# Kernel optimization log

Hardware: AMD Instinct MI355X
Metric: run time of the kernel (lower is better)

The kernel has to match this reference:

```python
import jax, jax.numpy as jnp
import numpy as np
from jax import lax

NX = 4096
NY = 4096
NLEVEL = 13  # int(log2(min(nx, ny))) + 1
OMEGA = 1.0
DN = ('NCHW', 'OIHW', 'NCHW')


def _bc(u):
    # torch boundary_condition: replicate edges into a zero-padded frame; corners stay 0
    up = jnp.pad(u, ((0, 0), (0, 0), (1, 1), (1, 1)), mode='edge')
    up = up.at[0, 0, 0, 0].set(0.0)
    up = up.at[0, 0, 0, -1].set(0.0)
    up = up.at[0, 0, -1, 0].set(0.0)
    up = up.at[0, 0, -1, -1].set(0.0)
    return up


def _prol(x):
    return jnp.repeat(jnp.repeat(x, 2, axis=2), 2, axis=3)


def setup_inputs() -> dict:
    key = jax.random.key(0)
    k1, k2 = jax.random.split(key)
    # realistic 5-point-like stencil with strong diagonal + randn perturbation
    base = jnp.array([[0.0, 1.0, 0.0], [1.0, 4.0, 1.0], [0.0, 1.0, 0.0]], dtype=jnp.float32)
    A = base + 0.01 * jax.random.normal(k1, (3, 3), dtype=jnp.float32)
    u0 = jax.random.normal(k2, (1, 1, NY, NX), dtype=jnp.float32)
    return {"A": A, "u0": u0, "t": 4}


def reference(A, u0, t):
    diag = A[1, 1]                      # center extracted before zeroing, as in __init__
    K = (A.at[1, 1].set(0.0))[None, None]  # (1,1,3,3) smoothing kernel, zero center
    KR = jnp.full((1, 1, 2, 2), 0.25, dtype=A.dtype)  # restriction kernel

    def smooth(x):
        return lax.conv_general_dilated(x, K, (1, 1), 'VALID', dimension_numbers=DN)

    def restrict(x):
        return lax.conv_general_dilated(x, KR, (2, 2), 'VALID', dimension_numbers=DN)

    b = 0.0
    u = u0
    for _ in range(t):
        r = smooth(_bc(u)) - b  # (1,1,NY,NX)
        r_s = [r]
        for _i in range(1, NLEVEL - 5):
            r = restrict(r)
            r_s.append(r)
        e = jnp.zeros((1, 1, 1, 1), dtype=A.dtype)
        for j in reversed(range(1, NLEVEL - 5)):
            e_pad = jnp.pad(e, ((0, 0), (0, 0), (1, 1), (1, 1)))
            e = e - smooth(e_pad) / diag + r_s[j] / diag  # broadcasts to r_s[j] shape
            e = _prol(e)
        u_update = u - e - smooth(_bc(u)) / diag + b / diag
        u = (1.0 - OMEGA) * u + OMEGA * u_update
    return (u - u.min()) / (u.max() - u.min())
```

## Files before the change

kernel.cpp:

```cpp
#include <hip/hip_runtime.h>

#define N 4096

__device__ __forceinline__ float bf2f(unsigned short h)
{
    unsigned int u = ((unsigned int)h) << 16;
    return __uint_as_float(u);
}
__device__ __forceinline__ unsigned short f2bf(float f)
{
    unsigned int x = __float_as_uint(f);
    unsigned int r = (x + 0x7FFFu + ((x >> 16) & 1u)) >> 16;
    return (unsigned short)r;
}

__device__ __forceinline__ int cr(int i) { return ((i + 1024) >> 1) - 512; }

__device__ __forceinline__ void load_A(const float* __restrict__ Ag,
                                       float Ac[3][3], float& inv)
{
#pragma unroll
    for (int i = 0; i < 9; ++i) Ac[i / 3][i % 3] = Ag[i];
    inv = 1.0f / Ac[1][1];
    Ac[1][1] = 0.f;
}

__device__ __forceinline__ void make_w44(const float Ac[3][3], float wt[4][4])
{
#pragma unroll
    for (int a = 0; a < 4; ++a)
#pragma unroll
        for (int b = 0; b < 4; ++b) wt[a][b] = 0.f;
#pragma unroll
    for (int r = 0; r < 2; ++r)
#pragma unroll
        for (int c = 0; c < 2; ++c)
#pragma unroll
            for (int i = 0; i < 3; ++i)
#pragma unroll
                for (int j = 0; j < 3; ++j) wt[r + i][c + j] += Ac[i][j];
}

template <typename TI>
__device__ __forceinline__ void load_row6T(const TI* __restrict__ u,
                                           int gy, int xm, int colL, int colR,
                                           bool cornL, bool cornR, bool yedge,
                                           float v[6])
{
    int cy = min(max(gy, 0), N - 1);
    const TI* rowp = &u[(size_t)cy * N];
    float L, R;
    if constexpr (sizeof(TI) == 4) {
        float4 m = *(const float4*)&rowp[xm];
        v[1] = m.x; v[2] = m.y; v[3] = m.z; v[4] = m.w;
        L = rowp[colL];
        R = rowp[colR];
    } else {
        ushort4 m = *(const ushort4*)&rowp[xm];
        v[1] = bf2f(m.x); v[2] = bf2f(m.y); v[3] = bf2f(m.z); v[4] = bf2f(m.w);
        L = bf2f(rowp[colL]);
        R = bf2f(rowp[colR]);
    }
    if (yedge) {
        bool oob = (gy < 0) | (gy >= N);
        if (oob & cornL) L = 0.f;
        if (oob & cornR) R = 0.f;
    }
    v[0] = L; v[5] = R;
}

__device__ __forceinline__ void swz2048(int bid, int& bx, int& by)
{
    int reg = (bid & 7) * 256 + (bid >> 3);
    bx = reg & 15;
    by = reg >> 4;
}

template <typename TI>
__global__ __launch_bounds__(256) void smooth_restrict2_kernel(
    const TI* __restrict__ u, const float* __restrict__ Ag,
    unsigned short* __restrict__ r2, float* __restrict__ r3)
{
    int t = threadIdx.x, lane = t & 63, w = t >> 6;
    int bx, by;
    swz2048(blockIdx.x, bx, by);
    int x0 = 256 * bx;
    int Y0 = 16 * by + 4 * w;
    int gy0 = 2 * Y0 - 1;
    bool yedge = (gy0 < 0) | (gy0 + 9 >= N);
    float Ac[3][3], inv;
    load_A(Ag, Ac, inv);
    float wt[4][4];
    make_w44(Ac, wt);

    int xm = x0 + 4 * lane;
    int colL = max(xm - 1, 0), colR = min(xm + 4, N - 1);
    bool cornL = (xm - 1 < 0), cornR = (xm + 4 >= N);
    float v[10][6];
#pragma unroll
    for (int rr = 0; rr < 10; ++rr)
        load_row6T<TI>(u, gy0 + rr, xm, colL, colR, cornL, cornR, yedge, v[rr]);

    float o0[4], o1[4];
#pragma unroll
    for (int q = 0; q < 4; ++q) {
        float a0 = 0.f, a1 = 0.f;
#pragma unroll
        for (int a = 0; a < 4; ++a) {
            const float* vv = v[2 * q + a];
#pragma unroll
            for (int b = 0; b < 4; ++b) {
                a0 += wt[a][b] * vv[b];
                a1 += wt[a][b] * vv[b + 2];
            }
        }
        o0[q] = 0.25f * a0;
        o1[q] = 0.25f * a1;
    }
    int Y2 = Y0 >> 1, X2 = 64 * bx + lane;
    float val0 = 0.25f * (o0[0] + o1[0] + o0[1] + o1[1]);
    float val1 = 0.25f * (o0[2] + o1[2] + o0[3] + o1[3]);
    r2[(size_t)Y2 * 1024 + X2] = f2bf(val0);
    r2[(size_t)(Y2 + 1) * 1024 + X2] = f2bf(val1);
    float s0 = val0 + val1;
    float s1 = __shfl_xor(s0, 1);
    if (!(lane & 1))
        r3[(size_t)(Y2 >> 1) * 512 + (X2 >> 1)] = 0.25f * (s0 + s1);
}

__global__ __launch_bounds__(256) void multirestrict_kernel(
    const float* __restrict__ r3, float* __restrict__ r4, float* __restrict__ r5,
    float* __restrict__ r6, float* __restrict__ r7)
{
    int BX = blockIdx.x, BY = blockIdx.y;
    __shared__ float s4[16][17];
    __shared__ float s5[8][9];
    __shared__ float s6[4][5];
    int t = threadIdx.x;
    {
        int y = t >> 4, x = t & 15;
        const float* b0 = &r3[(size_t)(32 * BY + 2 * y) * 512 + 32 * BX + 2 * x];
        float2 a = *(const float2*)b0;
        float2 b = *(const float2*)(b0 + 512);
        float vv = 0.25f * (a.x + a.y + b.x + b.y);
        r4[(size_t)(16 * BY + y) * 256 + 16 * BX + x] = vv;
        s4[y][x] = vv;
    }
    __syncthreads();
    if (t < 64) {
        int y = t >> 3, x = t & 7;
        float vv = 0.25f * (s4[2 * y][2 * x] + s4[2 * y][2 * x + 1] +
                            s4[2 * y + 1][2 * x] + s4[2 * y + 1][2 * x + 1]);
        r5[(size_t)(8 * BY + y) * 128 + 8 * BX + x] = vv;
        s5[y][x] = vv;
    }
    __syncthreads();
    if (t < 16) {
        int y = t >> 2, x = t & 3;
        float vv = 0.25f * (s5[2 * y][2 * x] + s5[2 * y][2 * x + 1] +
                            s5[2 * y + 1][2 * x] + s5[2 * y + 1][2 * x + 1]);
        r6[(size_t)(4 * BY + y) * 64 + 4 * BX + x] = vv;
        s6[y][x] = vv;
    }
    __syncthreads();
    if (t < 4) {
        int y = t >> 1, x = t & 1;
        float vv = 0.25f * (s6[2 * y][2 * x] + s6[2 * y][2 * x + 1] +
                            s6[2 * y + 1][2 * x] + s6[2 * y + 1][2 * x + 1]);
        r7[(size_t)(2 * BY + y) * 32 + 2 * BX + x] = vv;
    }
}

template <typename TI, typename TO, bool WANTMM>
__global__ __launch_bounds__(256) void final_fused_kernel(
    const TI* __restrict__ u,
    const float* __restrict__ r7, const float* __restrict__ r6,
    const float* __restrict__ r5, const float* __restrict__ r4,
    const float* __restrict__ r3, const unsigned short* __restrict__ r2,
    const float* __restrict__ Ag, TO* __restrict__ uo,
    float* __restrict__ partials)
{
    const int n = N;
    int t = threadIdx.x, lane = t & 63, w = t >> 6;
    int bx, by;
    swz2048(blockIdx.x, bx, by);
    int x0 = 256 * bx, y0 = 32 * by;
    __shared__ float s32p[3][4];
    __shared__ float s64p[3][6];
    __shared__ float s128p[3][10];
    __shared__ float s256p[4][18];
    __shared__ float s512v[6][36];
    __shared__ float s1024[10][68];
    float Ac[3][3], inv;
    load_A(Ag, Ac, inv);
    float wt[4][4];
    make_w44(Ac, wt);

    int yb = y0 + 8 * w;
    int gyu = yb - 1;
    bool yedge = (gyu < 0) | (gyu + 9 >= n);
    int xm = x0 + 4 * lane;
    int colL = max(xm - 1, 0), colR = min(xm + 4, n - 1);
    bool cornL = (xm - 1 < 0), cornR = (xm + 4 >= n);
    float v[10][6];
#pragma unroll
    for (int rr = 0; rr < 10; ++rr)
        load_row6T<TI>(u, gyu + rr, xm, colL, colR, cornL, cornR, yedge, v[rr]);

    int R32 = (by >> 2) - 1, C32 = 2 * bx - 1;
    if (t < 12) {
        int pr = t >> 2, pc = t & 3;
        int gy = R32 + pr, gx = C32 + pc;
        s32p[pr][pc] = (gy >= 0 && gy < 32 && gx >= 0 && gx < 32)
                           ? r7[(size_t)gy * 32 + gx] * inv : 0.f;
    }
    __syncthreads();
    int R64 = (by >> 1) - 1, C64 = 4 * bx - 1;
    if (t < 18) {
        int pr = t / 6, pc = t - (t / 6) * 6;
        int gy = R64 + pr, gx = C64 + pc;
        float val = 0.f;
        if (gy >= 0 && gy < 64 && gx >= 0 && gx < 64) {
            float ctr = s32p[cr(gy) - R32][cr(gx) - C32];
            float sm = 0.f;
#pragma unroll
            for (int dy = -1; dy <= 1; ++dy)
#pragma unroll
                for (int dx = -1; dx <= 1; ++dx) {
                    if (dy == 0 && dx == 0) continue;
                    sm += Ac[dy + 1][dx + 1] * s32p[cr(gy + dy) - R32][cr(gx + dx) - C32];
                }
            val = ctr - sm * inv + r6[(size_t)gy * 64 + gx] * inv;
        }
        s64p[pr][pc] = val;
    }
    __syncthreads();
    int R128 = by - 1, C128 = 8 * bx - 1;
    if (t < 30) {
        int pr = t / 10, pc = t - (t / 10) * 10;
        int gy = R128 + pr, gx = C128 + pc;
        float val = 0.f;
        if (gy >= 0 && gy < 128 && gx >= 0 && gx < 128) {
            float ctr = s64p[cr(gy) - R64][cr(gx) - C64];
            float sm = 0.f;
#pragma unroll
            for (int dy = -1; dy <= 1; ++dy)
#pragma unroll
                for (int dx = -1; dx <= 1; ++dx) {
                    if (dy == 0 && dx == 0) continue;
                    sm += Ac[dy + 1][dx + 1] * s64p[cr(gy + dy) - R64][cr(gx + dx) - C64];
                }
            val = ctr - sm * inv + r5[(size_t)gy * 128 + gx] * inv;
        }
        s128p[pr][pc] = val;
    }
    __syncthreads();
    int R256 = 2 * by - 1, C256 = 16 * bx - 1;
    if (t < 72) {
        int pr = t / 18, pc = t - (t / 18) * 18;
        int gy = R256 + pr, gx = C256 + pc;
        float val = 0.f;
        if (gy >= 0 && gy < 256 && gx >= 0 && gx < 256) {
            float ctr = s128p[cr(gy) - R128][cr(gx) - C128];
            float sm = 0.f;
#pragma unroll
            for (int dy = -1; dy <= 1; ++dy)
#pragma unroll
                for (int dx = -1; dx <= 1; ++dx) {
                    if (dy == 0 && dx == 0) continue;
                    sm += Ac[dy + 1][dx + 1] * s128p[cr(gy + dy) - R128][cr(gx + dx) - C128];
                }
            val = ctr - sm * inv + r4[(size_t)gy * 256 + gx] * inv;
        }
        s256p[pr][pc] = val;
    }
    __syncthreads();
    int S5r = 4 * by - 1, S5c = 32 * bx - 1;
    if (t < 216) {
        int pr = t / 36, pc = t - (t / 36) * 36;
        int gy = S5r + pr, gx = S5c + pc;
        float val = 0.f;
        if (pc < 34 && gy >= 0 && gy < 512 && gx >= 0 && gx < 512) {
            float ctr = s256p[cr(gy) - R256][cr(gx) - C256];
            float sm = 0.f;
#pragma unroll
            for (int dy = -1; dy <= 1; ++dy)
#pragma unroll
                for (int dx = -1; dx <= 1; ++dx) {
                    if (dy == 0 && dx == 0) continue;
                    sm += Ac[dy + 1][dx + 1] * s256p[cr(gy + dy) - R256][cr(gx + dx) - C256];
                }
            val = ctr - sm * inv + r3[(size_t)gy * 512 + gx] * inv;
        }
        s512v[pr][pc] = val;
    }
    __syncthreads();
    int R10 = 8 * by - 1, C10 = 64 * bx - 1;
    for (int i = t; i < 680; i += 256) {
        int pr = i / 68, pc = i - (i / 68) * 68;
        if (pc < 66) {
            int gy = R10 + pr, gx = C10 + pc;
            float val = 0.f;
            if (gy >= 0 && gy < 1024 && gx >= 0 && gx < 1024) {
                float ctr = s512v[cr(gy) - S5r][cr(gx) - S5c];
                float sm = 0.f;
#pragma unroll
                for (int dy = -1; dy <= 1; ++dy)
#pragma unroll
                    for (int dx = -1; dx <= 1; ++dx) {
                        if (dy == 0 && dx == 0) continue;
                        sm += Ac[dy + 1][dx + 1] *
                              s512v[cr(gy + dy) - S5r][cr(gx + dx) - S5c];
                    }
                val = ctr - sm * inv + bf2f(r2[(size_t)gy * 1024 + gx]) * inv;
            }
            s1024[pr][pc] = val;
        }
    }
    __syncthreads();
    float e2[4][2];
    int EY0 = 16 * by + 4 * w, EX0 = 128 * bx + 2 * lane;
#pragma unroll
    for (int a = 0; a < 4; ++a) {
        int gy = EY0 + a;
        float a0 = 0.f, a1 = 0.f;
#pragma unroll
        for (int i = 0; i < 4; ++i) {
            const float* vv = v[2 * a + i];
#pragma unroll
            for (int j = 0; j < 4; ++j) {
                a0 += wt[i][j] * vv[j];
                a1 += wt[i][j] * vv[j + 2];
            }
        }
        float r1v[2] = {0.25f * a0, 0.25f * a1};
#pragma unroll
        for (int b = 0; b < 2; ++b) {
            int gx = EX0 + b;
            float ctr = s1024[(gy >> 1) - R10][(gx >> 1) - C10];
            float sm = 0.f;
#pragma unroll
            for (int dy = -1; dy <= 1; ++dy)
#pragma unroll
                for (int dx = -1; dx <= 1; ++dx) {
                    if (dy == 0 && dx == 0) continue;
                    sm += Ac[dy + 1][dx + 1] *
                          s1024[((gy + dy) >> 1) - R10][((gx + dx) >> 1) - C10];
                }
            e2[a][b] = ctr - sm * inv + r1v[b] * inv;
        }
    }
    float mn = 3.402823466e+38f, mx = -3.402823466e+38f;
#pragma unroll
    for (int r = 0; r < 8; ++r) {
        int y = yb + r;
        const float* va = v[r];
        const float* vb = v[r + 1];
        const float* vc = v[r + 2];
        float out[4];
#pragma unroll
        for (int c = 0; c < 4; ++c) {
            float sm = Ac[0][0] * va[c] + Ac[0][1] * va[c + 1] + Ac[0][2] * va[c + 2]
                     + Ac[1][0] * vb[c]                        + Ac[1][2] * vb[c + 2]
                     + Ac[2][0] * vc[c] + Ac[2][1] * vc[c + 1] + Ac[2][2] * vc[c + 2];
            out[c] = vb[c + 1] - e2[r >> 1][c >> 1] - sm * inv;
        }
        if constexpr (sizeof(TO) == 4) {
            *(float4*)&uo[(size_t)y * n + xm] =
                make_float4(out[0], out[1], out[2], out[3]);
        } else {
            ushort4 o;
            o.x = f2bf(out[0]); o.y = f2bf(out[1]);
            o.z = f2bf(out[2]); o.w = f2bf(out[3]);
            *(ushort4*)&uo[(size_t)y * n + xm] = o;
        }
        if (WANTMM) {
            mn = fminf(mn, fminf(fminf(out[0], out[1]), fminf(out[2], out[3])));
            mx = fmaxf(mx, fmaxf(fmaxf(out[0], out[1]), fmaxf(out[2], out[3])));
        }
    }
    if (WANTMM) {
#pragma unroll
        for (int off = 32; off > 0; off >>= 1) {
            mn = fminf(mn, __shfl_down(mn, off));
            mx = fmaxf(mx, __shfl_down(mx, off));
        }
        __shared__ float smn[4], smx[4];
        if (lane == 0) { smn[w] = mn; smx[w] = mx; }
        __syncthreads();
        if (t == 0) {
            mn = smn[0]; mx = smx[0];
            for (int wq = 1; wq < 4; ++wq) { mn = fminf(mn, smn[wq]); mx = fmaxf(mx, smx[wq]); }
            int bid = by * 16 + bx;
            partials[2 * bid] = mn;
            partials[2 * bid + 1] = mx;
        }
    }
}

__global__ __launch_bounds__(1024) void minmax_final_kernel(
    const float* __restrict__ partials, float* __restrict__ mm)
{
    float mn = 3.402823466e+38f, mx = -3.402823466e+38f;
    for (int i = threadIdx.x; i < 2048; i += 1024) {
        mn = fminf(mn, partials[2 * i]);
        mx = fmaxf(mx, partials[2 * i + 1]);
    }
#pragma unroll
    for (int off = 32; off > 0; off >>= 1) {
        mn = fminf(mn, __shfl_down(mn, off));
        mx = fmaxf(mx, __shfl_down(mx, off));
    }
    __shared__ float smn[16], smx[16];
    int lane = threadIdx.x & 63, wv = threadIdx.x >> 6;
    if (lane == 0) { smn[wv] = mn; smx[wv] = mx; }
    __syncthreads();
    if (threadIdx.x == 0) {
        mn = smn[0]; mx = smx[0];
        for (int w = 1; w < 16; ++w) { mn = fminf(mn, smn[w]); mx = fmaxf(mx, smx[w]); }
        mm[0] = mn;
        mm[1] = mx;
    }
}

__global__ __launch_bounds__(256) void normalize_kernel(
    const unsigned short* __restrict__ uin, float* __restrict__ uout,
    const float* __restrict__ mm)
{
    size_t i = ((size_t)blockIdx.x * 256 + threadIdx.x) * 4;
    float mn = mm[0];
    float sc = 1.0f / (mm[1] - mm[0]);
    ushort4 h = *(const ushort4*)&uin[i];
    float4 v;
    v.x = (bf2f(h.x) - mn) * sc;
    v.y = (bf2f(h.y) - mn) * sc;
    v.z = (bf2f(h.z) - mn) * sc;
    v.w = (bf2f(h.w) - mn) * sc;
    *(float4*)&uout[i] = v;
}

extern "C" void kernel_launch(void* const* d_in, const int* in_sizes, int n_in,
                              void* d_out, int out_size, void* d_ws, size_t ws_size,
                              hipStream_t stream)
{
    const float* A  = (const float*)d_in[0];
    const float* u0 = (const float*)d_in[1];
    float* uout = (float*)d_out;
    char* ws = (char*)d_ws;

    size_t off = 0;
    auto alloc_f = [&](size_t nelem) { float* p = (float*)(ws + off); off += nelem * 4; return p; };
    float* r3 = alloc_f(512ull * 512);
    float* r4 = alloc_f(256ull * 256);
    float* r5 = alloc_f(128ull * 128);
    float* r6 = alloc_f(64ull * 64);
    float* r7 = alloc_f(32ull * 32);
    float* partials = alloc_f(4096);
    float* mm = alloc_f(2);
    off = (off + 15) & ~15ull;
    unsigned short* r2 = (unsigned short*)(ws + off); off += 1024ull * 1024 * 2;
    off = (off + 15) & ~15ull;
    unsigned short* ubA = (unsigned short*)(ws + off); off += 4096ull * 4096 * 2;
    unsigned short* ubB = (unsigned short*)(ws + off); off += 4096ull * 4096 * 2;

    for (int it = 0; it < 4; ++it) {
        if (it == 0) {
            smooth_restrict2_kernel<float><<<2048, 256, 0, stream>>>(u0, A, r2, r3);
        } else {
            const unsigned short* us = (it == 2) ? ubB : ubA;
            smooth_restrict2_kernel<unsigned short><<<2048, 256, 0, stream>>>(us, A, r2, r3);
        }
        multirestrict_kernel<<<dim3(16, 16), 256, 0, stream>>>(r3, r4, r5, r6, r7);
        if (it == 0) {
            final_fused_kernel<float, unsigned short, false><<<2048, 256, 0, stream>>>(
                u0, r7, r6, r5, r4, r3, r2, A, ubA, partials);
        } else if (it == 1) {
            final_fused_kernel<unsigned short, unsigned short, false><<<2048, 256, 0, stream>>>(
                ubA, r7, r6, r5, r4, r3, r2, A, ubB, partials);
        } else if (it == 2) {
            final_fused_kernel<unsigned short, unsigned short, false><<<2048, 256, 0, stream>>>(
                ubB, r7, r6, r5, r4, r3, r2, A, ubA, partials);
        } else {
            final_fused_kernel<unsigned short, unsigned short, true><<<2048, 256, 0, stream>>>(
                ubA, r7, r6, r5, r4, r3, r2, A, ubB, partials);
        }
    }
    minmax_final_kernel<<<1, 1024, 0, stream>>>(partials, mm);
    normalize_kernel<<<16384, 256, 0, stream>>>(ubB, uout, mm);
}
```

Baseline: 175.4 us.

## Fuse multi-level restriction into final kernel and merge minmax into normalize

Removes the separate multirestrict kernel: each final_fused block now loads a 48x64 halo tile of r3 into shared memory and recomputes r4..r7 locally, reading coarse residuals from LDS instead of global buffers. Also folds the single-block minmax reduction into the normalize kernel, where each block reduces the 2048 partials itself and then processes 8192 elements. The goal is to cut two kernel launches and their serialization per run. In exchange, every block does redundant restriction work, adds several more barriers, and uses more shared memory, which may lower occupancy.

New measurement: 182.5 us. 4.0% more time.

```diff
diff --git a/kernel.cpp b/kernel.cpp
--- a/kernel.cpp
+++ b/kernel.cpp
@@ -128,63 +128,21 @@
         r3[(size_t)(Y2 >> 1) * 512 + (X2 >> 1)] = 0.25f * (s0 + s1);
 }
 
-__global__ __launch_bounds__(256) void multirestrict_kernel(
-    const float* __restrict__ r3, float* __restrict__ r4, float* __restrict__ r5,
-    float* __restrict__ r6, float* __restrict__ r7)
-{
-    int BX = blockIdx.x, BY = blockIdx.y;
-    __shared__ float s4[16][17];
-    __shared__ float s5[8][9];
-    __shared__ float s6[4][5];
-    int t = threadIdx.x;
-    {
-        int y = t >> 4, x = t & 15;
-        const float* b0 = &r3[(size_t)(32 * BY + 2 * y) * 512 + 32 * BX + 2 * x];
-        float2 a = *(const float2*)b0;
-        float2 b = *(const float2*)(b0 + 512);
-        float vv = 0.25f * (a.x + a.y + b.x + b.y);
-        r4[(size_t)(16 * BY + y) * 256 + 16 * BX + x] = vv;
-        s4[y][x] = vv;
-    }
-    __syncthreads();
-    if (t < 64) {
-        int y = t >> 3, x = t & 7;
-        float vv = 0.25f * (s4[2 * y][2 * x] + s4[2 * y][2 * x + 1] +
-                            s4[2 * y + 1][2 * x] + s4[2 * y + 1][2 * x + 1]);
-        r5[(size_t)(8 * BY + y) * 128 + 8 * BX + x] = vv;
-        s5[y][x] = vv;
-    }
-    __syncthreads();
-    if (t < 16) {
-        int y = t >> 2, x = t & 3;
-        float vv = 0.25f * (s5[2 * y][2 * x] + s5[2 * y][2 * x + 1] +
-                            s5[2 * y + 1][2 * x] + s5[2 * y + 1][2 * x + 1]);
-        r6[(size_t)(4 * BY + y) * 64 + 4 * BX + x] = vv;
-        s6[y][x] = vv;
-    }
-    __syncthreads();
-    if (t < 4) {
-        int y = t >> 1, x = t & 1;
-        float vv = 0.25f * (s6[2 * y][2 * x] + s6[2 * y][2 * x + 1] +
-                            s6[2 * y + 1][2 * x] + s6[2 * y + 1][2 * x + 1]);
-        r7[(size_t)(2 * BY + y) * 32 + 2 * BX + x] = vv;
-    }
-}
-
 template <typename TI, typename TO, bool WANTMM>
 __global__ __launch_bounds__(256) void final_fused_kernel(
-    const TI* __restrict__ u,
-    const float* __restrict__ r7, const float* __restrict__ r6,
-    const float* __restrict__ r5, const float* __restrict__ r4,
-    const float* __restrict__ r3, const unsigned short* __restrict__ r2,
-    const float* __restrict__ Ag, TO* __restrict__ uo,
-    float* __restrict__ partials)
+    const TI* __restrict__ u, const float* __restrict__ r3,
+    const unsigned short* __restrict__ r2, const float* __restrict__ Ag,
+    TO* __restrict__ uo, float* __restrict__ partials)
 {
     const int n = N;
     int t = threadIdx.x, lane = t & 63, w = t >> 6;
     int bx, by;
     swz2048(blockIdx.x, bx, by);
     int x0 = 256 * bx, y0 = 32 * by;
+    __shared__ float sr3[48][66];
+    __shared__ float sr4[24][33];
+    __shared__ float sr5[12][17];
+    __shared__ float sr6[6][9];
     __shared__ float s32p[3][4];
     __shared__ float s64p[3][6];
     __shared__ float s128p[3][10];
@@ -207,12 +165,51 @@
     for (int rr = 0; rr < 10; ++rr)
         load_row6T<TI>(u, gyu + rr, xm, colL, colR, cornL, cornR, yedge, v[rr]);
 
+    int R3r = 16 * (by >> 2) - 16, R3c = 32 * bx - 16;
+    {
+        bool interior = (R3r >= 0) & (R3r + 48 <= 512) & (R3c >= 0) & (R3c + 64 <= 512);
+        if (interior) {
+            for (int i = t; i < 1536; i += 256) {
+                int rr = i >> 5, cc = (i & 31) * 2;
+                *(float2*)&sr3[rr][cc] =
+                    *(const float2*)&r3[(size_t)(R3r + rr) * 512 + R3c + cc];
+            }
+        } else {
+            for (int i = t; i < 3072; i += 256) {
+                int rr = i >> 6, cc = i & 63;
+                int gy = R3r + rr, gx = R3c + cc;
+                sr3[rr][cc] = (gy >= 0 && gy < 512 && gx >= 0 && gx < 512)
+                                  ? r3[(size_t)gy * 512 + gx] : 0.f;
+            }
+        }
+    }
+    __syncthreads();
+    int R4r = 8 * (by >> 2) - 8, R4c = 16 * bx - 8;
+    for (int i = t; i < 768; i += 256) {
+        int y = i >> 5, x = i & 31;
+        sr4[y][x] = 0.25f * (sr3[2 * y][2 * x] + sr3[2 * y][2 * x + 1] +
+                             sr3[2 * y + 1][2 * x] + sr3[2 * y + 1][2 * x + 1]);
+    }
+    __syncthreads();
+    int R5r = 4 * (by >> 2) - 4, R5c = 8 * bx - 4;
+    if (t < 192) {
+        int y = t >> 4, x = t & 15;
+        sr5[y][x] = 0.25f * (sr4[2 * y][2 * x] + sr4[2 * y][2 * x + 1] +
+                             sr4[2 * y + 1][2 * x] + sr4[2 * y + 1][2 * x + 1]);
+    }
+    __syncthreads();
+    int R6r = 2 * (by >> 2) - 2, R6c = 4 * bx - 2;
+    if (t < 48) {
+        int y = t >> 3, x = t & 7;
+        sr6[y][x] = 0.25f * (sr5[2 * y][2 * x] + sr5[2 * y][2 * x + 1] +
+                             sr5[2 * y + 1][2 * x] + sr5[2 * y + 1][2 * x + 1]);
+    }
+    __syncthreads();
     int R32 = (by >> 2) - 1, C32 = 2 * bx - 1;
     if (t < 12) {
-        int pr = t >> 2, pc = t & 3;
-        int gy = R32 + pr, gx = C32 + pc;
-        s32p[pr][pc] = (gy >= 0 && gy < 32 && gx >= 0 && gx < 32)
-                           ? r7[(size_t)gy * 32 + gx] * inv : 0.f;
+        int y = t >> 2, x = t & 3;
+        s32p[y][x] = 0.25f * (sr6[2 * y][2 * x] + sr6[2 * y][2 * x + 1] +
+                              sr6[2 * y + 1][2 * x] + sr6[2 * y + 1][2 * x + 1]) * inv;
     }
     __syncthreads();
     int R64 = (by >> 1) - 1, C64 = 4 * bx - 1;
@@ -230,7 +227,7 @@
                     if (dy == 0 && dx == 0) continue;
                     sm += Ac[dy + 1][dx + 1] * s32p[cr(gy + dy) - R32][cr(gx + dx) - C32];
                 }
-            val = ctr - sm * inv + r6[(size_t)gy * 64 + gx] * inv;
+            val = ctr - sm * inv + sr6[gy - R6r][gx - R6c] * inv;
         }
         s64p[pr][pc] = val;
     }
@@ -250,7 +247,7 @@
                     if (dy == 0 && dx == 0) continue;
                     sm += Ac[dy + 1][dx + 1] * s64p[cr(gy + dy) - R64][cr(gx + dx) - C64];
                 }
-            val = ctr - sm * inv + r5[(size_t)gy * 128 + gx] * inv;
+            val = ctr - sm * inv + sr5[gy - R5r][gx - R5c] * inv;
         }
         s128p[pr][pc] = val;
     }
@@ -270,7 +267,7 @@
                     if (dy == 0 && dx == 0) continue;
                     sm += Ac[dy + 1][dx + 1] * s128p[cr(gy + dy) - R128][cr(gx + dx) - C128];
                 }
-            val = ctr - sm * inv + r4[(size_t)gy * 256 + gx] * inv;
+            val = ctr - sm * inv + sr4[gy - R4r][gx - R4c] * inv;
         }
         s256p[pr][pc] = val;
     }
@@ -290,7 +287,7 @@
                     if (dy == 0 && dx == 0) continue;
                     sm += Ac[dy + 1][dx + 1] * s256p[cr(gy + dy) - R256][cr(gx + dx) - C256];
                 }
-            val = ctr - sm * inv + r3[(size_t)gy * 512 + gx] * inv;
+            val = ctr - sm * inv + sr3[gy - R3r][gx - R3c] * inv;
         }
         s512v[pr][pc] = val;
     }
@@ -398,11 +395,13 @@
     }
 }
 
-__global__ __launch_bounds__(1024) void minmax_final_kernel(
-    const float* __restrict__ partials, float* __restrict__ mm)
-{
+__global__ __launch_bounds__(256) void normalize_kernel(
+    const unsigned short* __restrict__ uin, float* __restrict__ uout,
+    const float* __restrict__ partials)
+{
+    int t = threadIdx.x, lane = t & 63, w = t >> 6;
     float mn = 3.402823466e+38f, mx = -3.402823466e+38f;
-    for (int i = threadIdx.x; i < 2048; i += 1024) {
+    for (int i = t; i < 2048; i += 256) {
         mn = fminf(mn, partials[2 * i]);
         mx = fmaxf(mx, partials[2 * i + 1]);
     }
@@ -411,32 +410,30 @@
         mn = fminf(mn, __shfl_down(mn, off));
         mx = fmaxf(mx, __shfl_down(mx, off));
     }
-    __shared__ float smn[16], smx[16];
-    int lane = threadIdx.x & 63, wv = threadIdx.x >> 6;
-    if (lane == 0) { smn[wv] = mn; smx[wv] = mx; }
-    __syncthreads();
-    if (threadIdx.x == 0) {
+    __shared__ float smn[4], smx[4];
+    __shared__ float mmv[2];
+    if (lane == 0) { smn[w] = mn; smx[w] = mx; }
+    __syncthreads();
+    if (t == 0) {
         mn = smn[0]; mx = smx[0];
-        for (int w = 1; w < 16; ++w) { mn = fminf(mn, smn[w]); mx = fmaxf(mx, smx[w]); }
-        mm[0] = mn;
-        mm[1] = mx;
-    }
-}
-
-__global__ __launch_bounds__(256) void normalize_kernel(
-    const unsigned short* __restrict__ uin, float* __restrict__ uout,
-    const float* __restrict__ mm)
-{
-    size_t i = ((size_t)blockIdx.x * 256 + threadIdx.x) * 4;
-    float mn = mm[0];
-    float sc = 1.0f / (mm[1] - mm[0]);
-    ushort4 h = *(const ushort4*)&uin[i];
-    float4 v;
-    v.x = (bf2f(h.x) - mn) * sc;
-    v.y = (bf2f(h.y) - mn) * sc;
-    v.z = (bf2f(h.z) - mn) * sc;
-    v.w = (bf2f(h.w) - mn) * sc;
-    *(float4*)&uout[i] = v;
+        for (int wq = 1; wq < 4; ++wq) { mn = fminf(mn, smn[wq]); mx = fmaxf(mx, smx[wq]); }
+        mmv[0] = mn;
+        mmv[1] = 1.0f / (mx - mn);
+    }
+    __syncthreads();
+    float mnv = mmv[0], sc = mmv[1];
+    size_t base = (size_t)blockIdx.x * 8192;
+#pragma unroll
+    for (int k = 0; k < 8; ++k) {
+        size_t i = base + (size_t)k * 1024 + t * 4;
+        ushort4 h = *(const ushort4*)&uin[i];
+        float4 o;
+        o.x = (bf2f(h.x) - mnv) * sc;
+        o.y = (bf2f(h.y) - mnv) * sc;
+        o.z = (bf2f(h.z) - mnv) * sc;
+        o.w = (bf2f(h.w) - mnv) * sc;
+        *(float4*)&uout[i] = o;
+    }
 }
 
 extern "C" void kernel_launch(void* const* d_in, const int* in_sizes, int n_in,
@@ -451,12 +448,7 @@
     size_t off = 0;
     auto alloc_f = [&](size_t nelem) { float* p = (float*)(ws + off); off += nelem * 4; return p; };
     float* r3 = alloc_f(512ull * 512);
-    float* r4 = alloc_f(256ull * 256);
-    float* r5 = alloc_f(128ull * 128);
-    float* r6 = alloc_f(64ull * 64);
-    float* r7 = alloc_f(32ull * 32);
     float* partials = alloc_f(4096);
-    float* mm = alloc_f(2);
     off = (off + 15) & ~15ull;
     unsigned short* r2 = (unsigned short*)(ws + off); off += 1024ull * 1024 * 2;
     off = (off + 15) & ~15ull;
@@ -470,21 +462,19 @@
             const unsigned short* us = (it == 2) ? ubB : ubA;
             smooth_restrict2_kernel<unsigned short><<<2048, 256, 0, stream>>>(us, A, r2, r3);
         }
-        multirestrict_kernel<<<dim3(16, 16), 256, 0, stream>>>(r3, r4, r5, r6, r7);
         if (it == 0) {
             final_fused_kernel<float, unsigned short, false><<<2048, 256, 0, stream>>>(
-                u0, r7, r6, r5, r4, r3, r2, A, ubA, partials);
+                u0, r3, r2, A, ubA, partials);
         } else if (it == 1) {
             final_fused_kernel<unsigned short, unsigned short, false><<<2048, 256, 0, stream>>>(
-                ubA, r7, r6, r5, r4, r3, r2, A, ubB, partials);
+                ubA, r3, r2, A, ubB, partials);
         } else if (it == 2) {
             final_fused_kernel<unsigned short, unsigned short, false><<<2048, 256, 0, stream>>>(
-                ubB, r7, r6, r5, r4, r3, r2, A, ubA, partials);
+                ubB, r3, r2, A, ubA, partials);
         } else {
             final_fused_kernel<unsigned short, unsigned short, true><<<2048, 256, 0, stream>>>(
-                ubA, r7, r6, r5, r4, r3, r2, A, ubB, partials);
-        }
-    }
-    minmax_final_kernel<<<1, 1024, 0, stream>>>(partials, mm);
-    normalize_kernel<<<16384, 256, 0, stream>>>(ubB, uout, mm);
-}
+                ubA, r3, r2, A, ubB, partials);
+        }
+    }
+    normalize_kernel<<<2048, 256, 0, stream>>>(ubB, uout, partials);
+}
```
